# Performance work log

Measured on AMD Instinct MI355X. Metric: run time of the kernel, lower is better.

The kernel has to match this reference:

```python
import jax, jax.numpy as jnp
import numpy as np


def _haar_dwt(x):
    # pywt 'haar' dwt2 on even-sized inputs: non-overlapping 2x2 blocks.
    # For block [[a,b],[c,d]]: cA=(a+b+c+d)/2, cH=(a+b-c-d)/2,
    # cV=(a-b+c-d)/2, cD=(a-b-c+d)/2  (pywt dec_hi = [-1/sqrt2, 1/sqrt2]).
    B, C, H, W = x.shape
    xb = x.reshape(B, C, H // 2, 2, W // 2, 2)
    a = xb[:, :, :, 0, :, 0]
    b = xb[:, :, :, 0, :, 1]
    c = xb[:, :, :, 1, :, 0]
    d = xb[:, :, :, 1, :, 1]
    ll = (a + b + c + d) * 0.5
    ch = (a + b - c - d) * 0.5
    cv = (a - b + c - d) * 0.5
    cd = (a - b - c + d) * 0.5
    return ll, ch, cv, cd


def _haar_idwt(ll, ch, cv, cd):
    a = (ll + ch + cv + cd) * 0.5
    b = (ll + ch - cv - cd) * 0.5
    c = (ll - ch + cv - cd) * 0.5
    d = (ll - ch - cv + cd) * 0.5
    B, C, h2, w2 = ll.shape
    top = jnp.stack([a, b], axis=-1)   # [B,C,h2,w2,2]
    bot = jnp.stack([c, d], axis=-1)   # [B,C,h2,w2,2]
    y = jnp.stack([top, bot], axis=-3)  # [B,C,h2,2,w2,2]
    return y.reshape(B, C, 2 * h2, 2 * w2)


def _conv2d(x, w, b, groups=1, pad=1):
    y = jax.lax.conv_general_dilated(
        x, w, window_strides=(1, 1), padding=[(pad, pad), (pad, pad)],
        dimension_numbers=('NCHW', 'OIHW', 'NCHW'), feature_group_count=groups)
    return y + b[None, :, None, None]


def setup_inputs() -> dict:
    key = jax.random.key(0)
    ks = jax.random.split(key, 7)
    B, C, H, W = 8, 64, 256, 256
    C4 = 4 * C
    x = jax.random.normal(ks[0], (B, C, H, W), dtype=jnp.float32)
    dw_w = jax.random.normal(ks[1], (C4, 1, 3, 3), dtype=jnp.float32) / 3.0
    dw_b = jax.random.normal(ks[2], (C4,), dtype=jnp.float32) * 0.01
    pw_w = jax.random.normal(ks[3], (C4, C4, 1, 1), dtype=jnp.float32) / float(np.sqrt(C4))
    pw_b = jax.random.normal(ks[4], (C4,), dtype=jnp.float32) * 0.01
    cv_w = jax.random.normal(ks[5], (C4, C4, 3, 3), dtype=jnp.float32) / float(3.0 * np.sqrt(C4))
    cv_b = jax.random.normal(ks[6], (C4,), dtype=jnp.float32) * 0.01
    return {"x": x, "dw_w": dw_w, "dw_b": dw_b, "pw_w": pw_w,
            "pw_b": pw_b, "cv_w": cv_w, "cv_b": cv_b}


def reference(x, dw_w, dw_b, pw_w, pw_b, cv_w, cv_b):
    B, C, H, W = x.shape  # source math requires H == W (spatial transpose)
    C4 = 4 * C
    ll, ch, cv, cd = _haar_dwt(x)
    # Source stores each subband spatially TRANSPOSED (transpose(2,1,0)).
    sub = jnp.stack([jnp.swapaxes(s, -1, -2) for s in (ll, ch, cv, cd)], axis=2)
    t = sub.reshape(B, C4, H // 2, W // 2)  # channel order c*4 + {LL,cH,cV,cD}
    t = _conv2d(t, dw_w, dw_b, groups=C4, pad=1)  # depthwise 3x3
    t = _conv2d(t, pw_w, pw_b, groups=1, pad=0)   # pointwise 1x1
    t = _conv2d(t, cv_w, cv_b, groups=1, pad=1)   # dense 3x3
    t = jax.nn.gelu(t, approximate=False)         # torch nn.GELU() = exact erf
    t = t.reshape(B, C, 4, H // 2, W // 2)
    # Inverse path un-transposes each subband (transpose(0,2) in source).
    ll2, ch2, cv2, cd2 = [jnp.swapaxes(t[:, :, k], -1, -2) for k in range(4)]
    return _haar_idwt(ll2, ch2, cv2, cd2)
```

## Files before the change

### kernel.cpp

```cpp
#include <hip/hip_runtime.h>
#include <hip/hip_bf16.h>

#define DEVI __device__ __forceinline__

typedef __attribute__((ext_vector_type(8))) short abf8;
typedef __attribute__((ext_vector_type(4))) float f32x4;

DEVI unsigned short f2bf(float f) {
  union { __hip_bfloat16 h; unsigned short u; } cvt;
  cvt.h = __float2bfloat16(f);
  return cvt.u;
}
DEVI float bf2f(unsigned short u) {
  return __uint_as_float(((unsigned)u) << 16);
}
DEVI void async16(const void* g, void* l) {
  __builtin_amdgcn_global_load_lds((__attribute__((address_space(1))) void*)(g),
                                   (__attribute__((address_space(3))) void*)(l), 16, 0, 0);
}

__global__ __launch_bounds__(256) void k0_prep(const float* __restrict__ pw_w,
                                               const float* __restrict__ cv_w,
                                               unsigned short* __restrict__ pwb,
                                               unsigned short* __restrict__ cvb) {
  int id = blockIdx.x * 256 + threadIdx.x;
  if (id < 65536) pwb[id] = f2bf(pw_w[id]);
  if (id < 589824) {
    int dd = id >> 16;
    int rem = id & 65535;
    cvb[id] = f2bf(cv_w[(size_t)rem * 9 + dd]);
  }
}

__global__ __launch_bounds__(256) void k1a_dwt(const float* __restrict__ x,
                                               unsigned short* __restrict__ t0) {
  __shared__ __align__(16) float L[64 * 65];
  const int t = threadIdx.x;
  const int u0 = (blockIdx.x & 3) * 32;
  const int v0 = (blockIdx.x >> 2) * 32;
  const int c = blockIdx.y, b = blockIdx.z;
  const float* xp = x + (((size_t)(b * 64 + c)) << 16);
  {
    const int row = t >> 2;
    const float* xr = xp + (size_t)(2 * v0 + row) * 256 + 2 * u0;
    float* Lr = L + row * 65;
    for (int j = 0; j < 4; ++j) {
      int col = ((t & 3) + j * 4) * 4;
      float4 val = *(const float4*)(xr + col);
      Lr[col] = val.x; Lr[col + 1] = val.y; Lr[col + 2] = val.z; Lr[col + 3] = val.w;
    }
  }
  __syncthreads();
  const int vv = t & 31;
  const int us = t >> 5;
  const size_t outc = ((size_t)(b * 256 + c * 4)) << 14;
  for (int pass = 0; pass < 4; ++pass) {
    int uu = us * 4 + pass;
    const float* Lp = L + (2 * vv) * 65 + 2 * uu;
    float a = Lp[0], bb = Lp[1], cc = Lp[65], dd = Lp[66];
    float sll = (a + bb + cc + dd) * 0.5f;
    float sch = (a + bb - cc - dd) * 0.5f;
    float scv = (a - bb + cc - dd) * 0.5f;
    float scd = (a - bb - cc + dd) * 0.5f;
    size_t base = outc + ((u0 + uu) << 7) + (v0 + vv);
    t0[base]         = f2bf(sll);
    t0[base + 16384] = f2bf(sch);
    t0[base + 32768] = f2bf(scv);
    t0[base + 49152] = f2bf(scd);
  }
}

__global__ __launch_bounds__(256) void k1b_dw(const unsigned short* __restrict__ t0,
                                              const float* __restrict__ dww,
                                              const float* __restrict__ dwb,
                                              unsigned short* __restrict__ t1) {
  __shared__ __align__(16) unsigned short S[32 * 181];
  __shared__ __align__(16) unsigned short O[128 * 32];
  const int t = threadIdx.x;
  const int u0 = (blockIdx.x >> 3) * 8;
  const int v0 = (blockIdx.x & 7) * 16;
  const int icB = blockIdx.y * 32;
  const int b = blockIdx.z;
  const unsigned short* t0b = t0 + (((size_t)(b * 256 + icB)) << 14);
  for (int idx = t; idx < 5760; idx += 256) {
    int ic = idx / 180;
    int r = idx - ic * 180;
    int uu = r / 18;
    int vvq = r - uu * 18;
    int gu = u0 + uu - 1, gv = v0 + vvq - 1;
    unsigned short val = 0;
    if ((unsigned)gu < 128u && (unsigned)gv < 128u)
      val = t0b[((size_t)ic << 14) + (gu << 7) + gv];
    S[ic * 181 + r] = val;
  }
  __syncthreads();
  const int icp = t & 15, uu = (t >> 4) & 7, vh = t >> 7;
  const int cc0 = icB + icp * 2;
  float w0[9], w1[9];
  const float* wp = dww + cc0 * 9;
  for (int i = 0; i < 9; ++i) { w0[i] = wp[i]; w1[i] = wp[9 + i]; }
  const float b0 = dwb[cc0], b1 = dwb[cc0 + 1];
  const unsigned short* S0 = S + (icp * 2) * 181 + uu * 18 + vh * 8;
  const unsigned short* S1 = S0 + 181;
  float a0[3][3], a1[3][3];
  for (int du = 0; du < 3; ++du)
    for (int dv = 0; dv < 2; ++dv) {
      a0[du][dv] = bf2f(S0[du * 18 + dv]);
      a1[du][dv] = bf2f(S1[du * 18 + dv]);
    }
  unsigned* O32 = (unsigned*)O;
  for (int vv = 0; vv < 8; ++vv) {
    for (int du = 0; du < 3; ++du) {
      a0[du][2] = bf2f(S0[du * 18 + vv + 2]);
      a1[du][2] = bf2f(S1[du * 18 + vv + 2]);
    }
    float s0 = b0, s1 = b1;
    for (int du = 0; du < 3; ++du)
      for (int dv = 0; dv < 3; ++dv) {
        s0 += w0[du * 3 + dv] * a0[du][dv];
        s1 += w1[du * 3 + dv] * a1[du][dv];
      }
    int p = uu * 16 + vh * 8 + vv;
    O32[p * 16 + icp] = (unsigned)f2bf(s0) | ((unsigned)f2bf(s1) << 16);
    for (int du = 0; du < 3; ++du) {
      a0[du][0] = a0[du][1]; a0[du][1] = a0[du][2];
      a1[du][0] = a1[du][1]; a1[du][1] = a1[du][2];
    }
  }
  __syncthreads();
  const int p = t >> 1, hf = t & 1;
  const int pu = p >> 4, pv = p & 15;
  size_t gp = (size_t)((u0 + pu) * 128 + (v0 + pv));
  const uint4* src = (const uint4*)(O + p * 32 + hf * 16);
  uint4* dst = (uint4*)(t1 + ((((size_t)b * 16384) + gp) << 8) + icB + hf * 16);
  dst[0] = src[0];
  dst[1] = src[1];
}

__global__ __launch_bounds__(256) void k2_pw(const unsigned short* __restrict__ t1,
                                             const unsigned short* __restrict__ pwb,
                                             const float* __restrict__ pw_bias,
                                             unsigned short* __restrict__ t2) {
  __shared__ __align__(16) char smem[34816];
  unsigned short* As = (unsigned short*)smem;
  unsigned short* Bs = (unsigned short*)(smem + 8192);
  unsigned short* Ost = (unsigned short*)smem;
  const int t = threadIdx.x;
  const int wv = t >> 6, ln = t & 63;
  const int p0 = blockIdx.x * 128;
  const int oc0 = blockIdx.y * 128;
  const int b = blockIdx.z;
  const unsigned short* t1b = t1 + ((size_t)b << 22);
  const int lrow = ln >> 2, lic = (ln & 3) << 3;
  const int q = ln >> 4, cl = ln & 15;
  f32x4 acc[2][8] = {};
  for (int ic0 = 0; ic0 < 256; ic0 += 32) {
    __syncthreads();
    for (int cpy = 0; cpy < 2; ++cpy) {
      int row = wv * 32 + cpy * 16 + lrow;
      async16(pwb + (((size_t)(oc0 + row)) << 8) + ic0 + lic,
              As + (wv * 32 + cpy * 16) * 32);
      async16(t1b + (((size_t)(p0 + row)) << 8) + ic0 + lic,
              Bs + (wv * 32 + cpy * 16) * 32);
    }
    __syncthreads();
    abf8 a0 = *(const abf8*)(As + (wv * 32 + cl) * 32 + q * 8);
    abf8 a1 = *(const abf8*)(As + (wv * 32 + 16 + cl) * 32 + q * 8);
    for (int nt = 0; nt < 8; ++nt) {
      abf8 bf = *(const abf8*)(Bs + (nt * 16 + cl) * 32 + q * 8);
      acc[0][nt] = __builtin_amdgcn_mfma_f32_16x16x32_bf16(a0, bf, acc[0][nt], 0, 0, 0);
      acc[1][nt] = __builtin_amdgcn_mfma_f32_16x16x32_bf16(a1, bf, acc[1][nt], 0, 0, 0);
    }
  }
  __syncthreads();
  for (int mt = 0; mt < 2; ++mt) {
    int ocr = wv * 32 + mt * 16 + q * 4;
    float bb0 = pw_bias[oc0 + ocr],     bb1 = pw_bias[oc0 + ocr + 1];
    float bb2 = pw_bias[oc0 + ocr + 2], bb3 = pw_bias[oc0 + ocr + 3];
    for (int nt = 0; nt < 8; ++nt) {
      int p = nt * 16 + cl;
      short4 pk;
      pk.x = (short)f2bf(acc[mt][nt][0] + bb0);
      pk.y = (short)f2bf(acc[mt][nt][1] + bb1);
      pk.z = (short)f2bf(acc[mt][nt][2] + bb2);
      pk.w = (short)f2bf(acc[mt][nt][3] + bb3);
      *(short4*)(Ost + p * 136 + ocr) = pk;
    }
  }
  __syncthreads();
  const int pr = t >> 1, hf = t & 1;
  const uint4* src = (const uint4*)(Ost + pr * 136 + hf * 64);
  uint4* dst = (uint4*)(t2 + (((size_t)(b * 16384 + p0 + pr)) << 8) + oc0 + hf * 64);
  for (int j = 0; j < 8; ++j) dst[j] = src[j];
}

__global__ __launch_bounds__(256) void k3_cv(const unsigned short* __restrict__ t2,
                                             const unsigned short* __restrict__ cvb,
                                             const float* __restrict__ cv_bias,
                                             const unsigned short* __restrict__ zp,
                                             unsigned short* __restrict__ t3) {
  __shared__ __align__(16) char smem[34816];
  unsigned short* As = (unsigned short*)smem;
  unsigned short* Bs = (unsigned short*)(smem + 8192);
  unsigned short* Ost = (unsigned short*)smem;
  const int t = threadIdx.x;
  const int wv = t >> 6, ln = t & 63;
  const int oc0 = blockIdx.x * 128;
  const int u = blockIdx.y;
  const int b = blockIdx.z;
  const unsigned short* t2b = t2 + ((size_t)b << 22);
  const int lrow = ln >> 2, lic = (ln & 3) << 3;
  const int q = ln >> 4, cl = ln & 15;
  f32x4 acc[2][8] = {};
  for (int dd = 0; dd < 9; ++dd) {
    const int du = dd / 3, dv = dd - 3 * du;
    const int us = u + du - 1;
    const bool uok = (unsigned)us < 128u;
    const unsigned short* wbase = cvb + ((size_t)dd << 16);
    for (int ic0 = 0; ic0 < 256; ic0 += 32) {
      __syncthreads();
      for (int cpy = 0; cpy < 2; ++cpy) {
        int row = wv * 32 + cpy * 16 + lrow;
        async16(wbase + (((size_t)(oc0 + row)) << 8) + ic0 + lic,
                As + (wv * 32 + cpy * 16) * 32);
        int vss = row + dv - 1;
        const unsigned short* g =
            (uok && (unsigned)vss < 128u)
                ? t2b + (((size_t)(us * 128 + vss)) << 8) + ic0 + lic
                : zp + lic;
        async16(g, Bs + (wv * 32 + cpy * 16) * 32);
      }
      __syncthreads();
      abf8 a0 = *(const abf8*)(As + (wv * 32 + cl) * 32 + q * 8);
      abf8 a1 = *(const abf8*)(As + (wv * 32 + 16 + cl) * 32 + q * 8);
      for (int nt = 0; nt < 8; ++nt) {
        abf8 bf = *(const abf8*)(Bs + (nt * 16 + cl) * 32 + q * 8);
        acc[0][nt] = __builtin_amdgcn_mfma_f32_16x16x32_bf16(a0, bf, acc[0][nt], 0, 0, 0);
        acc[1][nt] = __builtin_amdgcn_mfma_f32_16x16x32_bf16(a1, bf, acc[1][nt], 0, 0, 0);
      }
    }
  }
  __syncthreads();
  for (int mt = 0; mt < 2; ++mt) {
    int ocr = wv * 32 + mt * 16 + q * 4;
    for (int r = 0; r < 4; ++r) {
      float bias = cv_bias[oc0 + ocr + r];
      for (int nt = 0; nt < 8; ++nt) {
        float xv = acc[mt][nt][r] + bias;
        float u_ = 0.7978845608028654f * xv * (1.0f + 0.044715f * xv * xv);
        float e = __expf(-2.0f * fabsf(u_));
        float th = (1.0f - e) / (1.0f + e);
        th = (u_ >= 0.0f) ? th : -th;
        float g = 0.5f * xv * (1.0f + th);
        Ost[(ocr + r) * 136 + nt * 16 + cl] = f2bf(g);
      }
    }
  }
  __syncthreads();
  const int rr = t >> 1, hf = t & 1;
  const uint4* src = (const uint4*)(Ost + rr * 136 + hf * 64);
  uint4* dst = (uint4*)(t3 + ((size_t)(b * 256 + oc0 + rr) << 14) + (u << 7) + hf * 64);
  for (int j = 0; j < 8; ++j) dst[j] = src[j];
}

__global__ __launch_bounds__(256) void k4_idwt(const unsigned short* __restrict__ t3,
                                               float* __restrict__ out) {
  __shared__ __align__(16) unsigned short L[4 * 32 * 34];
  const int t = threadIdx.x;
  const int w20 = (blockIdx.x & 3) * 32;
  const int h20 = (blockIdx.x >> 2) * 32;
  const int c = blockIdx.y, b = blockIdx.z;
  const unsigned short* t3b = t3 + (((size_t)(b * 256 + c * 4)) << 14);
  {
    const int row = t >> 1, hf = t & 1;
    const int k = row >> 5, w2i = row & 31;
    const unsigned* g = (const unsigned*)(t3b + ((size_t)k << 14) + ((w20 + w2i) << 7) + h20 + hf * 16);
    unsigned* l = (unsigned*)(L + (k * 32 + w2i) * 34 + hf * 16);
    for (int j = 0; j < 8; ++j) l[j] = g[j];
  }
  __syncthreads();
  const int w2 = t & 31;
  const int h2b = t >> 5;
  float* ob = out + (((size_t)(b * 64 + c)) << 16);
  for (int pass = 0; pass < 4; ++pass) {
    int h2 = h2b + pass * 8;
    int off = w2 * 34 + h2;
    float ll = bf2f(L[off]);
    float ch = bf2f(L[off + 1088]);
    float cv = bf2f(L[off + 2176]);
    float cd = bf2f(L[off + 3264]);
    float A  = (ll + ch + cv + cd) * 0.5f;
    float Bv = (ll + ch - cv - cd) * 0.5f;
    float Cv = (ll - ch + cv - cd) * 0.5f;
    float D  = (ll - ch - cv + cd) * 0.5f;
    int hg = (h20 + h2) * 2, wg = (w20 + w2) * 2;
    *(float2*)(ob + (size_t)hg * 256 + wg)       = make_float2(A, Bv);
    *(float2*)(ob + (size_t)(hg + 1) * 256 + wg) = make_float2(Cv, D);
  }
}

extern "C" void kernel_launch(void* const* d_in, const int* in_sizes, int n_in,
                              void* d_out, int out_size, void* d_ws, size_t ws_size,
                              hipStream_t stream) {
  const float* x    = (const float*)d_in[0];
  const float* dw_w = (const float*)d_in[1];
  const float* dw_b = (const float*)d_in[2];
  const float* pw_w = (const float*)d_in[3];
  const float* pw_b = (const float*)d_in[4];
  const float* cv_w = (const float*)d_in[5];
  const float* cv_b = (const float*)d_in[6];
  char* ws = (char*)d_ws;
  unsigned short* pwb  = (unsigned short*)(ws + 4096);
  unsigned short* cvb  = (unsigned short*)(ws + 4096 + 131072);
  unsigned short* bufA = (unsigned short*)(ws + (size_t)(2u << 20));
  unsigned short* bufB = (unsigned short*)(ws + (size_t)(70u << 20));
  hipMemsetAsync(ws, 0, 4096, stream);
  k0_prep<<<2304, 256, 0, stream>>>(pw_w, cv_w, pwb, cvb);
  k1a_dwt<<<dim3(16, 64, 8), 256, 0, stream>>>(x, bufA);
  k1b_dw<<<dim3(128, 8, 8), 256, 0, stream>>>(bufA, dw_w, dw_b, bufB);
  k2_pw<<<dim3(128, 2, 8), 256, 0, stream>>>(bufB, pwb, pw_b, bufA);
  k3_cv<<<dim3(2, 128, 8), 256, 0, stream>>>(bufA, cvb, cv_b, (const unsigned short*)ws, bufB);
  k4_idwt<<<dim3(16, 64, 8), 256, 0, stream>>>(bufB, (float*)d_out);
}
```

Before: 603.0 us.

## Reuse input row across horizontal taps in 3x3 conv and swizzle LDS slots

The dense 3x3 conv now loads one padded input row (130 pixels, with zeroed halo entries in LDS) once per vertical tap, along with the weights for all three horizontal taps. Each staged tile then feeds three shifted MFMA passes, replacing nine separate staged loads. Vertically out-of-range rows are skipped entirely, which removes the global zero-pad buffer and its memset. Both GEMM kernels also XOR-rotate the 16-byte chunk slot per row in LDS to cut bank conflicts on the abf8 reads, at the cost of larger LDS staging in the conv.

```diff
diff --git a/kernel.cpp b/kernel.cpp
--- a/kernel.cpp
+++ b/kernel.cpp
@@ -151,23 +151,23 @@
   const int oc0 = blockIdx.y * 128;
   const int b = blockIdx.z;
   const unsigned short* t1b = t1 + ((size_t)b << 22);
-  const int lrow = ln >> 2, lic = (ln & 3) << 3;
   const int q = ln >> 4, cl = ln & 15;
+  const int lr = ln >> 2, sp = ln & 3;
+  const int sc = (sp - (lr >> 1)) & 3;
+  const int soff = ((q + (cl >> 1)) & 3) * 8;
   f32x4 acc[2][8] = {};
   for (int ic0 = 0; ic0 < 256; ic0 += 32) {
     __syncthreads();
     for (int cpy = 0; cpy < 2; ++cpy) {
-      int row = wv * 32 + cpy * 16 + lrow;
-      async16(pwb + (((size_t)(oc0 + row)) << 8) + ic0 + lic,
-              As + (wv * 32 + cpy * 16) * 32);
-      async16(t1b + (((size_t)(p0 + row)) << 8) + ic0 + lic,
-              Bs + (wv * 32 + cpy * 16) * 32);
+      int rb = wv * 32 + cpy * 16;
+      async16(pwb + (((size_t)(oc0 + rb + lr)) << 8) + ic0 + sc * 8, As + rb * 32);
+      async16(t1b + (((size_t)(p0 + rb + lr)) << 8) + ic0 + sc * 8, Bs + rb * 32);
     }
     __syncthreads();
-    abf8 a0 = *(const abf8*)(As + (wv * 32 + cl) * 32 + q * 8);
-    abf8 a1 = *(const abf8*)(As + (wv * 32 + 16 + cl) * 32 + q * 8);
+    abf8 a0 = *(const abf8*)(As + (wv * 32 + cl) * 32 + soff);
+    abf8 a1 = *(const abf8*)(As + (wv * 32 + 16 + cl) * 32 + soff);
     for (int nt = 0; nt < 8; ++nt) {
-      abf8 bf = *(const abf8*)(Bs + (nt * 16 + cl) * 32 + q * 8);
+      abf8 bf = *(const abf8*)(Bs + (nt * 16 + cl) * 32 + soff);
       acc[0][nt] = __builtin_amdgcn_mfma_f32_16x16x32_bf16(a0, bf, acc[0][nt], 0, 0, 0);
       acc[1][nt] = __builtin_amdgcn_mfma_f32_16x16x32_bf16(a1, bf, acc[1][nt], 0, 0, 0);
     }
@@ -197,11 +197,10 @@
 __global__ __launch_bounds__(256) void k3_cv(const unsigned short* __restrict__ t2,
                                              const unsigned short* __restrict__ cvb,
                                              const float* __restrict__ cv_bias,
-                                             const unsigned short* __restrict__ zp,
                                              unsigned short* __restrict__ t3) {
   __shared__ __align__(16) char smem[34816];
   unsigned short* As = (unsigned short*)smem;
-  unsigned short* Bs = (unsigned short*)(smem + 8192);
+  unsigned short* Bs = (unsigned short*)(smem + 24576);
   unsigned short* Ost = (unsigned short*)smem;
   const int t = threadIdx.x;
   const int wv = t >> 6, ln = t & 63;
@@ -209,34 +208,43 @@
   const int u = blockIdx.y;
   const int b = blockIdx.z;
   const unsigned short* t2b = t2 + ((size_t)b << 22);
-  const int lrow = ln >> 2, lic = (ln & 3) << 3;
   const int q = ln >> 4, cl = ln & 15;
+  const int lr = ln >> 2, sp = ln & 3;
+  const int scA = (sp - (lr >> 1)) & 3;
+  const int scB = (sp - ((1 + lr) >> 1)) & 3;
+  const int soffA = ((q + (cl >> 1)) & 3) * 8;
+  if (t < 32) ((unsigned*)Bs)[t < 16 ? t : (2064 + (t - 16))] = 0;
   f32x4 acc[2][8] = {};
-  for (int dd = 0; dd < 9; ++dd) {
-    const int du = dd / 3, dv = dd - 3 * du;
+  for (int du = 0; du < 3; ++du) {
     const int us = u + du - 1;
-    const bool uok = (unsigned)us < 128u;
-    const unsigned short* wbase = cvb + ((size_t)dd << 16);
+    if ((unsigned)us >= 128u) continue;
+    const unsigned short* trow = t2b + ((size_t)us << 15);
+    const unsigned short* wdu = cvb + (((size_t)(du * 3)) << 16);
     for (int ic0 = 0; ic0 < 256; ic0 += 32) {
       __syncthreads();
-      for (int cpy = 0; cpy < 2; ++cpy) {
-        int row = wv * 32 + cpy * 16 + lrow;
-        async16(wbase + (((size_t)(oc0 + row)) << 8) + ic0 + lic,
-                As + (wv * 32 + cpy * 16) * 32);
-        int vss = row + dv - 1;
-        const unsigned short* g =
-            (uok && (unsigned)vss < 128u)
-                ? t2b + (((size_t)(us * 128 + vss)) << 8) + ic0 + lic
-                : zp + lic;
-        async16(g, Bs + (wv * 32 + cpy * 16) * 32);
+      for (int g = wv; g < 32; g += 4) {
+        if (g < 24) {
+          int dv = g >> 3, ch = g & 7;
+          async16(wdu + (((size_t)dv) << 16) + (((size_t)(oc0 + ch * 16 + lr)) << 8) + ic0 + scA * 8,
+                  As + dv * 4096 + ch * 512);
+        } else {
+          int ch = g - 24;
+          async16(trow + (((size_t)(ch * 16 + lr)) << 8) + ic0 + scB * 8,
+                  Bs + 32 + ch * 512);
+        }
       }
       __syncthreads();
-      abf8 a0 = *(const abf8*)(As + (wv * 32 + cl) * 32 + q * 8);
-      abf8 a1 = *(const abf8*)(As + (wv * 32 + 16 + cl) * 32 + q * 8);
-      for (int nt = 0; nt < 8; ++nt) {
-        abf8 bf = *(const abf8*)(Bs + (nt * 16 + cl) * 32 + q * 8);
-        acc[0][nt] = __builtin_amdgcn_mfma_f32_16x16x32_bf16(a0, bf, acc[0][nt], 0, 0, 0);
-        acc[1][nt] = __builtin_amdgcn_mfma_f32_16x16x32_bf16(a1, bf, acc[1][nt], 0, 0, 0);
+      for (int dv = 0; dv < 3; ++dv) {
+        const unsigned short* Adv = As + dv * 4096;
+        abf8 a0 = *(const abf8*)(Adv + (wv * 32 + cl) * 32 + soffA);
+        abf8 a1 = *(const abf8*)(Adv + (wv * 32 + 16 + cl) * 32 + soffA);
+        const int slotB = ((q + ((cl + dv) >> 1)) & 3) * 8;
+        const unsigned short* Bbase = Bs + (cl + dv) * 32 + slotB;
+        for (int nt = 0; nt < 8; ++nt) {
+          abf8 bf = *(const abf8*)(Bbase + nt * 512);
+          acc[0][nt] = __builtin_amdgcn_mfma_f32_16x16x32_bf16(a0, bf, acc[0][nt], 0, 0, 0);
+          acc[1][nt] = __builtin_amdgcn_mfma_f32_16x16x32_bf16(a1, bf, acc[1][nt], 0, 0, 0);
+        }
       }
     }
   }
@@ -314,11 +322,10 @@
   unsigned short* cvb  = (unsigned short*)(ws + 4096 + 131072);
   unsigned short* bufA = (unsigned short*)(ws + (size_t)(2u << 20));
   unsigned short* bufB = (unsigned short*)(ws + (size_t)(70u << 20));
-  hipMemsetAsync(ws, 0, 4096, stream);
   k0_prep<<<2304, 256, 0, stream>>>(pw_w, cv_w, pwb, cvb);
   k1a_dwt<<<dim3(16, 64, 8), 256, 0, stream>>>(x, bufA);
   k1b_dw<<<dim3(128, 8, 8), 256, 0, stream>>>(bufA, dw_w, dw_b, bufB);
   k2_pw<<<dim3(128, 2, 8), 256, 0, stream>>>(bufB, pwb, pw_b, bufA);
-  k3_cv<<<dim3(2, 128, 8), 256, 0, stream>>>(bufA, cvb, cv_b, (const unsigned short*)ws, bufB);
+  k3_cv<<<dim3(2, 128, 8), 256, 0, stream>>>(bufA, cvb, cv_b, bufB);
   k4_idwt<<<dim3(16, 64, 8), 256, 0, stream>>>(bufB, (float*)d_out);
 }
```

Measured after the change: 565.1 us. 6.3% less time.
